# Performance work log

Hardware: AMD Instinct MI355X
Metric: run time of the kernel (lower is better)

## Reference

```python
import jax, jax.numpy as jnp
import numpy as np

B, FRAMES, NBINS, HOP = 4, 400, 129, 240
T = FRAMES * HOP  # 96000


def hann_window(K, dtype=jnp.float32):
    # torch.hann_window default is periodic=True: 0.5*(1 - cos(2*pi*n/K))
    n = jnp.arange(K, dtype=dtype)
    return 0.5 - 0.5 * jnp.cos(2.0 * jnp.pi * n / K)


def get_minimum_phase_fir(log_mag):
    # log_mag: [B, F, NBINS] -> full spectrum [B, F, N], N = 2*(NBINS-1)
    full = jnp.concatenate([log_mag, jnp.flip(log_mag, -1)[..., 1:-1]], axis=-1)
    N = full.shape[-1]
    # Hilbert transform (scipy-style analytic signal), N even
    Xf = jnp.fft.fft(full, axis=-1)
    h = jnp.concatenate([
        jnp.ones((1,), full.dtype),
        2.0 * jnp.ones((N // 2 - 1,), full.dtype),
        jnp.ones((1,), full.dtype),
        jnp.zeros((N // 2 - 1,), full.dtype),
    ])
    analytic = jnp.fft.ifft(Xf * h, axis=-1)
    min_phase = -jnp.imag(analytic)
    freq_resp = jnp.exp(full + 1j * min_phase)
    return jnp.real(jnp.fft.ifft(freq_resp, axis=-1))  # [B, F, N]


def windowing(kernel):
    K = kernel.shape[-1]
    w = hann_window(K, kernel.dtype)
    w = w.at[: K // 2].set(1.0)
    return kernel * w


def upsample_linear(x, scale):
    # x: [B, K, L] -> [B, K, L*scale], matches F.upsample(mode='linear', align_corners=False)
    L = x.shape[-1]
    out = jnp.arange(L * scale, dtype=x.dtype)
    src = jnp.clip((out + 0.5) / scale - 0.5, 0.0, L - 1.0)
    lo = jnp.floor(src).astype(jnp.int32)
    hi = jnp.minimum(lo + 1, L - 1)
    w = src - lo.astype(x.dtype)
    return x[..., lo] * (1.0 - w) + x[..., hi] * w


def fir_filt(x, h):
    # x: [B, T], h: [B, T, K]; causal time-varying FIR: y[t] = sum_k h[t,k] * x[t-k]
    K = h.shape[-1]
    Tn = x.shape[-1]
    x_pad = jnp.pad(x, ((0, 0), (K - 1, 0)))
    idx = jnp.arange(Tn)[:, None] + jnp.arange(K)[None, :]  # [T, K]
    frames = x_pad[:, idx]  # [B, T, K] (im2col-like gather)
    return jnp.einsum('btk,btk->bt', frames, jnp.flip(h, -1))


def setup_inputs() -> dict:
    key = jax.random.key(0)
    k1, k2 = jax.random.split(key)
    ex = jax.random.normal(k1, (B, T), dtype=jnp.float32)
    log_mag = jax.random.normal(k2, (B, FRAMES, NBINS), dtype=jnp.float32)
    return {"ex": ex, "log_mag": log_mag, "hop_length": HOP}


def reference(ex, log_mag, hop_length):
    kernel = get_minimum_phase_fir(log_mag)          # [B, F, K]
    kernel = windowing(kernel)
    up = upsample_linear(jnp.transpose(kernel, (0, 2, 1)), hop_length)  # [B, K, F*hop]
    up = jnp.transpose(up, (0, 2, 1))                # [B, F*hop, K]
    Tn = min(ex.shape[1], up.shape[1])
    ex = ex[:, :Tn]
    up = up[:, :Tn]
    return fir_filt(ex, up)
```

## Files before the change

### kernel.cpp

```cpp
#include <hip/hip_runtime.h>
#include <math.h>

#define NB 4
#define FRAMES 400
#define NBINS 129
#define HOP 240
#define T_LEN (FRAMES * HOP)
#define KLEN 256

__global__ __launch_bounds__(128) void gen_fir(const float* __restrict__ log_mag,
                                               float* __restrict__ kern) {
    const int bf = blockIdx.x;
    const int n  = threadIdx.x;

    __shared__ __align__(16) float  full[132];
    __shared__ __align__(16) float  g[128];
    __shared__ __align__(16) float2 crci[128];

    const float* lm = log_mag + bf * NBINS;
    full[n] = lm[n];
    if (n == 0) full[128] = lm[128];

    float sa, ca;
    sincosf((float)n * 0.02454369260617026f , &sa, &ca);
    const float a2  = 2.0f * ca;
    const float sgn = (n & 1) ? -1.0f : 1.0f;
    __syncthreads();

    const float full0 = full[0];
    const float full128 = full[128];

    {
        const float4* f4p = (const float4*)full;
        float cm1 = ca, cm = 1.0f, acc = 0.0f;
#pragma unroll 8
        for (int u = 0; u < 32; ++u) {
            const float4 f4 = f4p[u];
            acc = fmaf(f4.x, cm, acc); { const float cn = fmaf(a2, cm, -cm1); cm1 = cm; cm = cn; }
            acc = fmaf(f4.y, cm, acc); { const float cn = fmaf(a2, cm, -cm1); cm1 = cm; cm = cn; }
            acc = fmaf(f4.z, cm, acc); { const float cn = fmaf(a2, cm, -cm1); cm1 = cm; cm = cn; }
            acc = fmaf(f4.w, cm, acc); { const float cn = fmaf(a2, cm, -cm1); cm1 = cm; cm = cn; }
        }
        const float Xf = 2.0f * acc - full0 + sgn * full128;
        g[n] = Xf * (1.0f / 128.0f);
    }
    __syncthreads();

    {
        const float4* g4p = (const float4*)g;
        float sm1 = -sa, sm = 0.0f, acc = 0.0f;
#pragma unroll 8
        for (int u = 0; u < 32; ++u) {
            const float4 gv = g4p[u];
            acc = fmaf(gv.x, sm, acc); { const float sn = fmaf(a2, sm, -sm1); sm1 = sm; sm = sn; }
            acc = fmaf(gv.y, sm, acc); { const float sn = fmaf(a2, sm, -sm1); sm1 = sm; sm = sn; }
            acc = fmaf(gv.z, sm, acc); { const float sn = fmaf(a2, sm, -sm1); sm1 = sm; sm = sn; }
            acc = fmaf(gv.w, sm, acc); { const float sn = fmaf(a2, sm, -sm1); sm1 = sm; sm = sn; }
        }
        const float mp = -acc;
        const float e  = expf(full[n]);
        float smp, cmp_;
        sincosf(mp, &smp, &cmp_);
        const float sc = (n == 0) ? 1.0f : 2.0f;
        crci[n] = make_float2(sc * e * cmp_, sc * e * smp);
    }
    __syncthreads();

    {
        const float e128 = expf(full128);
        const float4* cc4 = (const float4*)crci;
        float cm1 = ca, cm = 1.0f;
        float sm1 = -sa, sm = 0.0f;
        float accE = 0.0f, accO = 0.0f;
#pragma unroll 8
        for (int u = 0; u < 64; ++u) {
            const float4 q = cc4[u];
            accE = fmaf(q.x, cm, accE); accE = fmaf(-q.y, sm, accE);
            { const float cn = fmaf(a2, cm, -cm1); cm1 = cm; cm = cn;
              const float sn = fmaf(a2, sm, -sm1); sm1 = sm; sm = sn; }
            accO = fmaf(q.z, cm, accO); accO = fmaf(-q.w, sm, accO);
            { const float cn = fmaf(a2, cm, -cm1); cm1 = cm; cm = cn;
              const float sn = fmaf(a2, sm, -sm1); sm1 = sm; sm = sn; }
        }
        const float base = sgn * e128;
        const float k0 = (accE + accO + base) * (1.0f / 256.0f);
        const float k1 = (accE - accO + base) * (1.0f / 256.0f) * (0.5f + 0.5f * ca);
        kern[bf * KLEN + n]       = k0;
        kern[bf * KLEN + n + 128] = k1;
    }
}

__global__ __launch_bounds__(256) void fir_apply(const float* __restrict__ ex,
                                                 const float* __restrict__ kern,
                                                 float* __restrict__ out) {
    const int b   = blockIdx.y;
    const int t0  = blockIdx.x * 512;
    const int tid = threadIdx.x;

    __shared__ __align__(16) float  xs[768];
    __shared__ __align__(16) float2 kp[4][258];

    for (int i = tid; i < 768; i += 256) {
        const int t = t0 - 255 + i;
        xs[i] = (t >= 0 && t < T_LEN) ? ex[b * T_LEN + t] : 0.0f;
    }

    float src0 = ((float)t0 + 0.5f) * (1.0f / HOP) - 0.5f;
    src0 = fminf(fmaxf(src0, 0.0f), (float)(FRAMES - 1));
    const int f0 = (int)src0;
    const float* kb = kern + b * FRAMES * KLEN;
    for (int i = tid; i < 4 * 256; i += 256) {
        const int q = i >> 8, j = i & 255;
        const int fl = min(f0 + q,     FRAMES - 1);
        const int fh = min(f0 + q + 1, FRAMES - 1);
        kp[q][j] = make_float2(kb[fl * KLEN + j], kb[fh * KLEN + j]);
    }
    __syncthreads();

    const int te = t0 + 2 * tid;
    float se = ((float)te + 0.5f) * (1.0f / HOP) - 0.5f;
    se = fminf(fmaxf(se, 0.0f), (float)(FRAMES - 1));
    float so = ((float)te + 1.5f) * (1.0f / HOP) - 0.5f;
    so = fminf(fmaxf(so, 0.0f), (float)(FRAMES - 1));
    const int   lo = (int)se;
    const float we = se - (float)lo;
    const float wo = so - (float)lo;

    const float4* kq4 = (const float4*)&kp[lo - f0][0];

    const int base = 2 * tid;
    float carry = xs[base + 256];
    float aeL = 0.0f, aeH = 0.0f, aoL = 0.0f, aoH = 0.0f;
#pragma unroll 8
    for (int u = 0; u < 128; ++u) {
        const float2 v  = *(const float2*)&xs[base + 254 - 2 * u];
        const float4 k4 = kq4[u];
        aeL = fmaf(v.y,   k4.x, aeL);  aeH = fmaf(v.y,   k4.y, aeH);
        aoL = fmaf(carry, k4.x, aoL);  aoH = fmaf(carry, k4.y, aoH);
        aeL = fmaf(v.x,   k4.z, aeL);  aeH = fmaf(v.x,   k4.w, aeH);
        aoL = fmaf(v.y,   k4.z, aoL);  aoH = fmaf(v.y,   k4.w, aoH);
        carry = v.x;
    }

    if (te < T_LEN)     out[b * T_LEN + te]     = (1.0f - we) * aeL + we * aeH;
    if (te + 1 < T_LEN) out[b * T_LEN + te + 1] = (1.0f - wo) * aoL + wo * aoH;
}

extern "C" void kernel_launch(void* const* d_in, const int* in_sizes, int n_in,
                              void* d_out, int out_size, void* d_ws, size_t ws_size,
                              hipStream_t stream) {
    const float* ex      = (const float*)d_in[0];
    const float* log_mag = (const float*)d_in[1];
    float* kern = (float*)d_ws;
    float* out  = (float*)d_out;

    gen_fir<<<NB * FRAMES, 128, 0, stream>>>(log_mag, kern);

    dim3 grid((T_LEN + 511) / 512, NB);
    fir_apply<<<grid, 256, 0, stream>>>(ex, kern, out);
}
```

Measured before the change: 24.67 us.

## Align FIR blocks to frame segments and read kernel taps directly from global

fir_apply now gives each block one interpolation segment, the 240 samples between two frame centers, so every thread shares the same pair of frames. The kernel taps are read straight from global/L1 as float4 instead of staged into interleaved shared memory, and stores become float2. gen_fir swaps sincosf/expf for the hardware sin/cos/exp2 intrinsics with range reduction to cut transcendental cost. This launches more, smaller blocks (401x4 with 128 threads), and the intrinsics lose some accuracy compared with the library calls.

```diff
diff --git a/kernel.cpp b/kernel.cpp
--- a/kernel.cpp
+++ b/kernel.cpp
@@ -7,6 +7,9 @@
 #define HOP 240
 #define T_LEN (FRAMES * HOP)
 #define KLEN 256
+
+#define REC_C { const float cn = fmaf(a2, cm, -cm1); cm1 = cm; cm = cn; }
+#define REC_S { const float sn = fmaf(a2, sm, -sm1); sm1 = sm; sm = sn; }
 
 __global__ __launch_bounds__(128) void gen_fir(const float* __restrict__ log_mag,
                                                float* __restrict__ kern) {
@@ -21,13 +24,14 @@
     full[n] = lm[n];
     if (n == 0) full[128] = lm[128];
 
-    float sa, ca;
-    sincosf((float)n * 0.02454369260617026f , &sa, &ca);
+    const float rev_n = (float)n * (1.0f / 256.0f);
+    const float ca = __builtin_amdgcn_cosf(rev_n);
+    const float sa = __builtin_amdgcn_sinf(rev_n);
     const float a2  = 2.0f * ca;
     const float sgn = (n & 1) ? -1.0f : 1.0f;
     __syncthreads();
 
-    const float full0 = full[0];
+    const float full0   = full[0];
     const float full128 = full[128];
 
     {
@@ -36,10 +40,10 @@
 #pragma unroll 8
         for (int u = 0; u < 32; ++u) {
             const float4 f4 = f4p[u];
-            acc = fmaf(f4.x, cm, acc); { const float cn = fmaf(a2, cm, -cm1); cm1 = cm; cm = cn; }
-            acc = fmaf(f4.y, cm, acc); { const float cn = fmaf(a2, cm, -cm1); cm1 = cm; cm = cn; }
-            acc = fmaf(f4.z, cm, acc); { const float cn = fmaf(a2, cm, -cm1); cm1 = cm; cm = cn; }
-            acc = fmaf(f4.w, cm, acc); { const float cn = fmaf(a2, cm, -cm1); cm1 = cm; cm = cn; }
+            acc = fmaf(f4.x, cm, acc); REC_C;
+            acc = fmaf(f4.y, cm, acc); REC_C;
+            acc = fmaf(f4.z, cm, acc); REC_C;
+            acc = fmaf(f4.w, cm, acc); REC_C;
         }
         const float Xf = 2.0f * acc - full0 + sgn * full128;
         g[n] = Xf * (1.0f / 128.0f);
@@ -52,22 +56,24 @@
 #pragma unroll 8
         for (int u = 0; u < 32; ++u) {
             const float4 gv = g4p[u];
-            acc = fmaf(gv.x, sm, acc); { const float sn = fmaf(a2, sm, -sm1); sm1 = sm; sm = sn; }
-            acc = fmaf(gv.y, sm, acc); { const float sn = fmaf(a2, sm, -sm1); sm1 = sm; sm = sn; }
-            acc = fmaf(gv.z, sm, acc); { const float sn = fmaf(a2, sm, -sm1); sm1 = sm; sm = sn; }
-            acc = fmaf(gv.w, sm, acc); { const float sn = fmaf(a2, sm, -sm1); sm1 = sm; sm = sn; }
+            acc = fmaf(gv.x, sm, acc); REC_S;
+            acc = fmaf(gv.y, sm, acc); REC_S;
+            acc = fmaf(gv.z, sm, acc); REC_S;
+            acc = fmaf(gv.w, sm, acc); REC_S;
         }
         const float mp = -acc;
-        const float e  = expf(full[n]);
-        float smp, cmp_;
-        sincosf(mp, &smp, &cmp_);
+        const float e  = __builtin_amdgcn_exp2f(full[n] * 1.4426950408889634f);
+        float rev = mp * 0.15915494309189535f;
+        rev = rev - floorf(rev);
+        const float smp  = __builtin_amdgcn_sinf(rev);
+        const float cmp_ = __builtin_amdgcn_cosf(rev);
         const float sc = (n == 0) ? 1.0f : 2.0f;
         crci[n] = make_float2(sc * e * cmp_, sc * e * smp);
     }
     __syncthreads();
 
     {
-        const float e128 = expf(full128);
+        const float e128 = __builtin_amdgcn_exp2f(full128 * 1.4426950408889634f);
         const float4* cc4 = (const float4*)crci;
         float cm1 = ca, cm = 1.0f;
         float sm1 = -sa, sm = 0.0f;
@@ -76,74 +82,74 @@
         for (int u = 0; u < 64; ++u) {
             const float4 q = cc4[u];
             accE = fmaf(q.x, cm, accE); accE = fmaf(-q.y, sm, accE);
-            { const float cn = fmaf(a2, cm, -cm1); cm1 = cm; cm = cn;
-              const float sn = fmaf(a2, sm, -sm1); sm1 = sm; sm = sn; }
+            REC_C; REC_S;
             accO = fmaf(q.z, cm, accO); accO = fmaf(-q.w, sm, accO);
-            { const float cn = fmaf(a2, cm, -cm1); cm1 = cm; cm = cn;
-              const float sn = fmaf(a2, sm, -sm1); sm1 = sm; sm = sn; }
+            REC_C; REC_S;
         }
         const float base = sgn * e128;
-        const float k0 = (accE + accO + base) * (1.0f / 256.0f);
-        const float k1 = (accE - accO + base) * (1.0f / 256.0f) * (0.5f + 0.5f * ca);
-        kern[bf * KLEN + n]       = k0;
-        kern[bf * KLEN + n + 128] = k1;
+        const float s = 1.0f / 256.0f;
+        kern[bf * KLEN + n]       = (accE + accO + base) * s;
+        kern[bf * KLEN + n + 128] = (accE - accO + base) * s * (0.5f + 0.5f * ca);
     }
 }
 
-__global__ __launch_bounds__(256) void fir_apply(const float* __restrict__ ex,
+__global__ __launch_bounds__(128) void fir_apply(const float* __restrict__ ex,
                                                  const float* __restrict__ kern,
                                                  float* __restrict__ out) {
     const int b   = blockIdx.y;
-    const int t0  = blockIdx.x * 512;
+    const int bs  = blockIdx.x;
     const int tid = threadIdx.x;
 
-    __shared__ __align__(16) float  xs[768];
-    __shared__ __align__(16) float2 kp[4][258];
+    const int start = (bs == 0) ? 0 : 240 * bs - 120;
+    const int end   = min(T_LEN, 240 * bs + 120);
+    const int f     = (bs == 0) ? 0 : bs - 1;
+    const int fh    = min(f + 1, FRAMES - 1);
 
-    for (int i = tid; i < 768; i += 256) {
-        const int t = t0 - 255 + i;
-        xs[i] = (t >= 0 && t < T_LEN) ? ex[b * T_LEN + t] : 0.0f;
-    }
+    __shared__ float xs[496];
 
-    float src0 = ((float)t0 + 0.5f) * (1.0f / HOP) - 0.5f;
-    src0 = fminf(fmaxf(src0, 0.0f), (float)(FRAMES - 1));
-    const int f0 = (int)src0;
-    const float* kb = kern + b * FRAMES * KLEN;
-    for (int i = tid; i < 4 * 256; i += 256) {
-        const int q = i >> 8, j = i & 255;
-        const int fl = min(f0 + q,     FRAMES - 1);
-        const int fh = min(f0 + q + 1, FRAMES - 1);
-        kp[q][j] = make_float2(kb[fl * KLEN + j], kb[fh * KLEN + j]);
+    const float* xb = ex + b * T_LEN;
+    for (int i = tid; i < 496; i += 128) {
+        const int t = start - 255 + i;
+        xs[i] = (t >= 0 && t < T_LEN) ? xb[t] : 0.0f;
     }
     __syncthreads();
 
-    const int te = t0 + 2 * tid;
+    const int te = start + 2 * tid;
+    if (te >= end) return;
+
     float se = ((float)te + 0.5f) * (1.0f / HOP) - 0.5f;
     se = fminf(fmaxf(se, 0.0f), (float)(FRAMES - 1));
     float so = ((float)te + 1.5f) * (1.0f / HOP) - 0.5f;
     so = fminf(fmaxf(so, 0.0f), (float)(FRAMES - 1));
-    const int   lo = (int)se;
-    const float we = se - (float)lo;
-    const float wo = so - (float)lo;
+    const float we = se - (float)f;
+    const float wo = so - (float)f;
 
-    const float4* kq4 = (const float4*)&kp[lo - f0][0];
+    const float* kL = kern + (b * FRAMES + f)  * KLEN;
+    const float* kH = kern + (b * FRAMES + fh) * KLEN;
 
     const int base = 2 * tid;
     float carry = xs[base + 256];
     float aeL = 0.0f, aeH = 0.0f, aoL = 0.0f, aoH = 0.0f;
-#pragma unroll 8
-    for (int u = 0; u < 128; ++u) {
-        const float2 v  = *(const float2*)&xs[base + 254 - 2 * u];
-        const float4 k4 = kq4[u];
-        aeL = fmaf(v.y,   k4.x, aeL);  aeH = fmaf(v.y,   k4.y, aeH);
-        aoL = fmaf(carry, k4.x, aoL);  aoH = fmaf(carry, k4.y, aoH);
-        aeL = fmaf(v.x,   k4.z, aeL);  aeH = fmaf(v.x,   k4.w, aeH);
-        aoL = fmaf(v.y,   k4.z, aoL);  aoH = fmaf(v.y,   k4.w, aoH);
-        carry = v.x;
+#pragma unroll 4
+    for (int u = 0; u < 64; ++u) {
+        const float2 v1 = *(const float2*)&xs[base + 254 - 4 * u];
+        const float2 v0 = *(const float2*)&xs[base + 252 - 4 * u];
+        const float4 kl4 = *(const float4*)(kL + 4 * u);
+        const float4 kh4 = *(const float4*)(kH + 4 * u);
+        aeL = fmaf(v1.y,  kl4.x, aeL); aeH = fmaf(v1.y,  kh4.x, aeH);
+        aoL = fmaf(carry, kl4.x, aoL); aoH = fmaf(carry, kh4.x, aoH);
+        aeL = fmaf(v1.x,  kl4.y, aeL); aeH = fmaf(v1.x,  kh4.y, aeH);
+        aoL = fmaf(v1.y,  kl4.y, aoL); aoH = fmaf(v1.y,  kh4.y, aoH);
+        aeL = fmaf(v0.y,  kl4.z, aeL); aeH = fmaf(v0.y,  kh4.z, aeH);
+        aoL = fmaf(v1.x,  kl4.z, aoL); aoH = fmaf(v1.x,  kh4.z, aoH);
+        aeL = fmaf(v0.x,  kl4.w, aeL); aeH = fmaf(v0.x,  kh4.w, aeH);
+        aoL = fmaf(v0.y,  kl4.w, aoL); aoH = fmaf(v0.y,  kh4.w, aoH);
+        carry = v0.x;
     }
 
-    if (te < T_LEN)     out[b * T_LEN + te]     = (1.0f - we) * aeL + we * aeH;
-    if (te + 1 < T_LEN) out[b * T_LEN + te + 1] = (1.0f - wo) * aoL + wo * aoH;
+    const float y0 = aeL + we * (aeH - aeL);
+    const float y1 = aoL + wo * (aoH - aoL);
+    *(float2*)(out + b * T_LEN + te) = make_float2(y0, y1);
 }
 
 extern "C" void kernel_launch(void* const* d_in, const int* in_sizes, int n_in,
@@ -156,6 +162,6 @@
 
     gen_fir<<<NB * FRAMES, 128, 0, stream>>>(log_mag, kern);
 
-    dim3 grid((T_LEN + 511) / 512, NB);
-    fir_apply<<<grid, 256, 0, stream>>>(ex, kern, out);
+    dim3 grid(401, NB);
+    fir_apply<<<grid, 128, 0, stream>>>(ex, kern, out);
 }
```

New measurement: 25.95 us. 5.2% more time.
